# Performance work log

Hardware: AMD Instinct MI355X
Metric: run time of the kernel (lower is better)

The kernel has to match this reference:

```python
import jax, jax.numpy as jnp
import numpy as np

OUT_DIM = 4096
DPC = 16
N = OUT_DIM * DPC  # 65536
BATCH = 512


def setup_inputs() -> dict:
    key = jax.random.key(0)
    k1, k2 = jax.random.split(key)
    x = jax.random.normal(k1, (BATCH, N), dtype=jnp.float32)
    duty_cycle = jax.random.uniform(k2, (N,), dtype=jnp.float32)
    boost_strength = jnp.ones((1,), dtype=jnp.float32)
    return {"x": x, "duty_cycle": duty_cycle, "boost_strength": boost_strength}


def reference(x, duty_cycle, boost_strength):
    # GenericKWinners.forward in training mode (k = out_dim), boost_strength > 0.
    n = x.shape[1]
    target_density = OUT_DIM / n
    bs = boost_strength[0]
    boost_factors = jnp.exp((target_density - duty_cycle) * bs)  # [N]
    # x is detached in the original before boosting/masking
    boosted = jax.lax.stop_gradient(x) * boost_factors  # [B, N]
    # Overlapping windows: group k covers [k*(dpc-1), k*(dpc-1)+dpc)
    starts = jnp.arange(OUT_DIM) * (DPC - 1)  # [OUT_DIM]
    win_idx = starts[:, None] + jnp.arange(DPC)[None, :]  # [OUT_DIM, DPC]
    windows = boosted[:, win_idx]  # [B, OUT_DIM, DPC]
    ind = jnp.argmax(windows, axis=-1)  # [B, OUT_DIM]
    mask = jax.nn.one_hot(ind, DPC, dtype=x.dtype)  # [B, OUT_DIM, DPC]
    mask = mask.reshape(x.shape[0], OUT_DIM * DPC)  # [B, N]
    return mask * x
```

## Files before the change

kernel.cpp:

```cpp
#include <hip/hip_runtime.h>

#define OUT_DIM 4096
#define DPC     16
#define NCOL    65536
#define BATCH   512
#define NWAVE   32768

__global__ void boost_table_kernel(const float* __restrict__ duty,
                                   const float* __restrict__ bs_ptr,
                                   float* __restrict__ bf) {
    int p = blockIdx.x * blockDim.x + threadIdx.x;
    if (p < NCOL) {
        float t = (0.0625f - duty[p]) * bs_ptr[0];
        bf[p] = (float)exp((double)t);
    }
}

__global__ __launch_bounds__(256, 8) void dkw_kernel(const float* __restrict__ x,
                                                     const float* __restrict__ bf,
                                                     float* __restrict__ out) {
    __shared__ float sb[4][1024];
    __shared__ int   sj[4][64];
    __shared__ float sv[4][64];

    const int lane = threadIdx.x & 63;
    const int wv   = threadIdx.x >> 6;
    const int gw   = blockIdx.x * 4 + wv;
    const int row  = gw >> 6;
    const int wc   = gw & 63;
    const int rowbase = row << 16;

    const int in_off = wc * 960;
    const float4* __restrict__ xg = (const float4*)(x + rowbase + in_off);
    const float4* __restrict__ bg = (const float4*)(bf + in_off);
    float4* __restrict__ sb4 = (float4*)sb[wv];
    #pragma unroll
    for (int r = 0; r < 4; ++r) {
        const int i = lane + 64 * r;
        float4 a = xg[i];
        float4 b = bg[i];
        float4 p;
        p.x = a.x * b.x; p.y = a.y * b.y; p.z = a.z * b.z; p.w = a.w * b.w;
        sb4[i] = p;
    }
    __threadfence_block();

    {
        const float* __restrict__ p = sb[wv] + lane * 15;
        float best = p[0];
        int   bj   = 0;
        #pragma unroll
        for (int k = 1; k < DPC; ++k) {
            float v = p[k];
            if (v > best) { best = v; bj = k; }
        }
        sj[wv][lane] = bj;
        sv[wv][lane] = x[rowbase + ((wc * 64 + lane) << 4) + bj];
    }
    __threadfence_block();

    float4* __restrict__ og = (float4*)(out + rowbase + (wc << 10));
    #pragma unroll
    for (int r = 0; r < 4; ++r) {
        const int i  = lane + 64 * r;
        const int w  = i >> 2;
        const int jm = sj[wv][w];
        const float val = sv[wv][w];
        const int j0 = (i & 3) << 2;
        float4 o;
        o.x = (j0     == jm) ? val : 0.0f;
        o.y = (j0 + 1 == jm) ? val : 0.0f;
        o.z = (j0 + 2 == jm) ? val : 0.0f;
        o.w = (j0 + 3 == jm) ? val : 0.0f;
        og[i] = o;
    }
}

extern "C" void kernel_launch(void* const* d_in, const int* in_sizes, int n_in,
                              void* d_out, int out_size, void* d_ws, size_t ws_size,
                              hipStream_t stream) {
    const float* x    = (const float*)d_in[0];
    const float* duty = (const float*)d_in[1];
    const float* bs   = (const float*)d_in[2];
    float* out = (float*)d_out;
    float* bf  = (float*)d_ws;

    hipLaunchKernelGGL(boost_table_kernel, dim3(NCOL / 256), dim3(256), 0, stream,
                       duty, bs, bf);
    hipLaunchKernelGGL(dkw_kernel, dim3(NWAVE / 4), dim3(256), 0, stream,
                       x, bf, out);
}
```

Baseline: 239.6 us.

## Replace LDS-staged wave kernel with per-thread register windows and nontemporal stores

Each thread now handles one output group directly. It loads its overlapping 15-stride window as five float4 loads of x and the boost table, does the argmax in registers, and writes its own 16 output values with four nontemporal float4 stores. This removes the shared-memory staging, the intra-wave fences and the scattered re-read of x. In exchange, adjacent threads' loads overlap and are strided rather than perfectly coalesced, and each thread also reads the x group it outputs, which adds redundant load traffic that must come from cache.

```diff
diff --git a/kernel.cpp b/kernel.cpp
--- a/kernel.cpp
+++ b/kernel.cpp
@@ -4,7 +4,10 @@
 #define DPC     16
 #define NCOL    65536
 #define BATCH   512
-#define NWAVE   32768
+#define TPB     256
+#define NBLK    ((BATCH * OUT_DIM) / TPB)
+
+typedef float nvec4 __attribute__((ext_vector_type(4)));
 
 __global__ void boost_table_kernel(const float* __restrict__ duty,
                                    const float* __restrict__ bs_ptr,
@@ -19,61 +22,55 @@
 __global__ __launch_bounds__(256, 8) void dkw_kernel(const float* __restrict__ x,
                                                      const float* __restrict__ bf,
                                                      float* __restrict__ out) {
-    __shared__ float sb[4][1024];
-    __shared__ int   sj[4][64];
-    __shared__ float sv[4][64];
+    const int g  = blockIdx.x * TPB + threadIdx.x;
+    const int r  = g >> 12;
+    const int wr = g & 4095;
+    const int f  = wr * 15;
+    const int b4 = f >> 2;
+    const int sh = f & 3;
+    const int o4 = wr << 2;
 
-    const int lane = threadIdx.x & 63;
-    const int wv   = threadIdx.x >> 6;
-    const int gw   = blockIdx.x * 4 + wv;
-    const int row  = gw >> 6;
-    const int wc   = gw & 63;
-    const int rowbase = row << 16;
+    const float4* __restrict__ xr = (const float4*)x + (r << 14);
+    const float4* __restrict__ br = (const float4*)bf;
 
-    const int in_off = wc * 960;
-    const float4* __restrict__ xg = (const float4*)(x + rowbase + in_off);
-    const float4* __restrict__ bg = (const float4*)(bf + in_off);
-    float4* __restrict__ sb4 = (float4*)sb[wv];
-    #pragma unroll
-    for (int r = 0; r < 4; ++r) {
-        const int i = lane + 64 * r;
-        float4 a = xg[i];
-        float4 b = bg[i];
-        float4 p;
-        p.x = a.x * b.x; p.y = a.y * b.y; p.z = a.z * b.z; p.w = a.w * b.w;
-        sb4[i] = p;
+    const float4 xa0 = xr[b4 + 0], xa1 = xr[b4 + 1], xa2 = xr[b4 + 2],
+                 xa3 = xr[b4 + 3], xa4 = xr[b4 + 4];
+    const float4 xo0 = xr[o4 + 0], xo1 = xr[o4 + 1],
+                 xo2 = xr[o4 + 2], xo3 = xr[o4 + 3];
+    const float4 qa0 = br[b4 + 0], qa1 = br[b4 + 1], qa2 = br[b4 + 2],
+                 qa3 = br[b4 + 3], qa4 = br[b4 + 4];
+
+    float best = -__builtin_inff();
+    int   bj   = 0;
+    #define STEP(xc, qc, d)                                        \
+    {                                                              \
+        const float bv = (xc) * (qc);                              \
+        const int   jj = (d) - sh;                                 \
+        if (((unsigned)jj < 16u) && (bv > best)) {                 \
+            best = bv; bj = jj;                                    \
+        }                                                          \
     }
-    __threadfence_block();
+    STEP(xa0.x, qa0.x,  0) STEP(xa0.y, qa0.y,  1) STEP(xa0.z, qa0.z,  2) STEP(xa0.w, qa0.w,  3)
+    STEP(xa1.x, qa1.x,  4) STEP(xa1.y, qa1.y,  5) STEP(xa1.z, qa1.z,  6) STEP(xa1.w, qa1.w,  7)
+    STEP(xa2.x, qa2.x,  8) STEP(xa2.y, qa2.y,  9) STEP(xa2.z, qa2.z, 10) STEP(xa2.w, qa2.w, 11)
+    STEP(xa3.x, qa3.x, 12) STEP(xa3.y, qa3.y, 13) STEP(xa3.z, qa3.z, 14) STEP(xa3.w, qa3.w, 15)
+    STEP(xa4.x, qa4.x, 16) STEP(xa4.y, qa4.y, 17) STEP(xa4.z, qa4.z, 18) STEP(xa4.w, qa4.w, 19)
+    #undef STEP
 
-    {
-        const float* __restrict__ p = sb[wv] + lane * 15;
-        float best = p[0];
-        int   bj   = 0;
-        #pragma unroll
-        for (int k = 1; k < DPC; ++k) {
-            float v = p[k];
-            if (v > best) { best = v; bj = k; }
-        }
-        sj[wv][lane] = bj;
-        sv[wv][lane] = x[rowbase + ((wc * 64 + lane) << 4) + bj];
-    }
-    __threadfence_block();
-
-    float4* __restrict__ og = (float4*)(out + rowbase + (wc << 10));
-    #pragma unroll
-    for (int r = 0; r < 4; ++r) {
-        const int i  = lane + 64 * r;
-        const int w  = i >> 2;
-        const int jm = sj[wv][w];
-        const float val = sv[wv][w];
-        const int j0 = (i & 3) << 2;
-        float4 o;
-        o.x = (j0     == jm) ? val : 0.0f;
-        o.y = (j0 + 1 == jm) ? val : 0.0f;
-        o.z = (j0 + 2 == jm) ? val : 0.0f;
-        o.w = (j0 + 3 == jm) ? val : 0.0f;
-        og[i] = o;
-    }
+    float4* __restrict__ og = (float4*)out + (r << 14) + o4;
+    float4 o;
+    o.x = (bj ==  0) ? xo0.x : 0.0f;  o.y = (bj ==  1) ? xo0.y : 0.0f;
+    o.z = (bj ==  2) ? xo0.z : 0.0f;  o.w = (bj ==  3) ? xo0.w : 0.0f;
+    __builtin_nontemporal_store(*(const nvec4*)&o, (nvec4*)&og[0]);
+    o.x = (bj ==  4) ? xo1.x : 0.0f;  o.y = (bj ==  5) ? xo1.y : 0.0f;
+    o.z = (bj ==  6) ? xo1.z : 0.0f;  o.w = (bj ==  7) ? xo1.w : 0.0f;
+    __builtin_nontemporal_store(*(const nvec4*)&o, (nvec4*)&og[1]);
+    o.x = (bj ==  8) ? xo2.x : 0.0f;  o.y = (bj ==  9) ? xo2.y : 0.0f;
+    o.z = (bj == 10) ? xo2.z : 0.0f;  o.w = (bj == 11) ? xo2.w : 0.0f;
+    __builtin_nontemporal_store(*(const nvec4*)&o, (nvec4*)&og[2]);
+    o.x = (bj == 12) ? xo3.x : 0.0f;  o.y = (bj == 13) ? xo3.y : 0.0f;
+    o.z = (bj == 14) ? xo3.z : 0.0f;  o.w = (bj == 15) ? xo3.w : 0.0f;
+    __builtin_nontemporal_store(*(const nvec4*)&o, (nvec4*)&og[3]);
 }
 
 extern "C" void kernel_launch(void* const* d_in, const int* in_sizes, int n_in,
@@ -87,6 +84,6 @@
 
     hipLaunchKernelGGL(boost_table_kernel, dim3(NCOL / 256), dim3(256), 0, stream,
                        duty, bs, bf);
-    hipLaunchKernelGGL(dkw_kernel, dim3(NWAVE / 4), dim3(256), 0, stream,
+    hipLaunchKernelGGL(dkw_kernel, dim3(NBLK), dim3(TPB), 0, stream,
                        x, bf, out);
 }
```

Measured after the change: 371.9 us. 1.55x slower.
